# Kernel tuning notes

Hardware: AMD Instinct MI355X
Metric: run time of the kernel (lower is better)

Reference implementation:

```python
import jax, jax.numpy as jnp
import numpy as np

NKV = 8      # n_head_kv
G = 8        # n_head // n_head_kv
D = 64       # head_dim (hardcoded in source views)
NH = NKV * G # n_head = 64


def rotate_half(x):
    x1, x2 = x[..., : D // 2], x[..., D // 2:]
    return jnp.concatenate((-x2, x1), axis=-1)


def setup_inputs() -> dict:
    key = jax.random.key(0)
    ks = jax.random.split(key, 9)
    B, S, H = 2, 1024, 4096
    hidden_states = jax.random.normal(ks[0], (B, S, H), dtype=jnp.float32)
    alibi = jnp.zeros((B * NH, 1, S), dtype=jnp.float32)            # unused in this forward path
    attention_mask = jnp.zeros((B, 1, S, S), dtype=jnp.float32)      # unused (is_causal=True)
    cos = jax.random.uniform(ks[1], (S, D), dtype=jnp.float32, minval=-1.0, maxval=1.0)
    sin = jax.random.uniform(ks[2], (S, D), dtype=jnp.float32, minval=-1.0, maxval=1.0)
    wq = jax.random.normal(ks[3], (H, H), dtype=jnp.float32) * 0.02          # Linear weight (out, in)
    wk = jax.random.normal(ks[4], (NKV * D, H), dtype=jnp.float32) * 0.02
    wv = jax.random.normal(ks[5], (NKV * D, H), dtype=jnp.float32) * 0.02
    wd = jax.random.normal(ks[6], (H, H), dtype=jnp.float32) * 0.02          # dense weight
    return {"hidden_states": hidden_states, "alibi": alibi, "attention_mask": attention_mask,
            "cos": cos, "sin": sin, "wq": wq, "wk": wk, "wv": wv, "wd": wd}


def reference(hidden_states, alibi, attention_mask, cos, sin, wq, wk, wv, wd):
    B, S, H = hidden_states.shape
    # fused-style projections (Linear: x @ W.T, no bias)
    # q: [B, S, NKV, G, D] -> [B, NKV, G, S, D]; head h = kv_group*G + j (group-major, matches source rearrange)
    q = (hidden_states @ wq.T).reshape(B, S, NKV, G, D).transpose(0, 2, 3, 1, 4)
    k = (hidden_states @ wk.T).reshape(B, S, NKV, D).transpose(0, 2, 1, 3)   # [B, NKV, S, D]
    v = (hidden_states @ wv.T).reshape(B, S, NKV, D).transpose(0, 2, 1, 3)
    # RoPE (cos/sin broadcast over batch/head dims)
    q = q * cos + rotate_half(q) * sin
    k = k * cos + rotate_half(k) * sin
    # grouped-query attention without materializing broadcast K/V
    inv_norm = jnp.asarray(1.0 / np.sqrt(D), dtype=hidden_states.dtype)
    scores = jnp.einsum('bkgsd,bktd->bkgst', q, k) * inv_norm        # [B, NKV, G, S, S]
    causal = jnp.tril(jnp.ones((S, S), dtype=bool))
    neg = jnp.finfo(scores.dtype).min
    scores = jnp.where(causal, scores, scores + neg)
    probs = jax.nn.softmax(scores, axis=-1)
    out = jnp.einsum('bkgst,bktd->bkgsd', probs, v)                  # [B, NKV, G, S, D]
    out = out.reshape(B, NH, S, D).transpose(0, 2, 1, 3).reshape(B, S, NH * D)
    return out @ wd.T
```

## Files before the change

### kernel.cpp

```cpp
#include <hip/hip_runtime.h>
#include <hip/hip_bf16.h>
#include <cstdint>

typedef short short8 __attribute__((ext_vector_type(8)));
typedef __bf16 bf16x8 __attribute__((ext_vector_type(8)));
typedef float float4v __attribute__((ext_vector_type(4)));
typedef float float16v __attribute__((ext_vector_type(16)));

#define NKV 8
#define G 8
#define D 64
#define NH 64
#define BB 2
#define S 1024
#define H 4096
#define MROWS (BB*S)
#define NQKV (H + 2*NKV*D)

__device__ __forceinline__ unsigned short f2b(float f) {
    union { float f; uint32_t u; } v; v.f = f;
    uint32_t u = v.u;
    uint32_t r = (u + 0x7FFFu + ((u >> 16) & 1u)) >> 16;
    return (unsigned short)r;
}
__device__ __forceinline__ float b2f(unsigned short b) {
    union { float f; uint32_t u; } v; v.u = ((uint32_t)b) << 16;
    return v.f;
}

__device__ __forceinline__ void gload_lds16(const unsigned short* g, unsigned short* l) {
    __builtin_amdgcn_global_load_lds(
        (const __attribute__((address_space(1))) uint32_t*)g,
        (__attribute__((address_space(3))) uint32_t*)l, 16, 0, 0);
}

__global__ void cvt_all(const float* __restrict__ hs, const float* __restrict__ wq,
                        const float* __restrict__ wk, const float* __restrict__ wv,
                        const float* __restrict__ wd,
                        unsigned short* __restrict__ hs_b, unsigned short* __restrict__ wqkv_b,
                        unsigned short* __restrict__ wd_b) {
    const size_t N0 = (size_t)MROWS * H;
    const size_t N1 = (size_t)H * H;
    const size_t N2 = (size_t)512 * H;
    const size_t N3 = (size_t)512 * H;
    const size_t N4 = (size_t)H * H;
    const size_t total4 = (N0 + N1 + N2 + N3 + N4) / 4;
    size_t i = (size_t)blockIdx.x * blockDim.x + threadIdx.x;
    const size_t stride = (size_t)gridDim.x * blockDim.x;
    for (; i < total4; i += stride) {
        size_t e = i * 4;
        const float* s; unsigned short* d;
        if (e < N0)                { s = hs + e;                  d = hs_b + e; }
        else if (e < N0+N1)        { s = wq + (e-N0);             d = wqkv_b + (e-N0); }
        else if (e < N0+N1+N2)     { s = wk + (e-N0-N1);          d = wqkv_b + N1 + (e-N0-N1); }
        else if (e < N0+N1+N2+N3)  { s = wv + (e-N0-N1-N2);       d = wqkv_b + N1+N2 + (e-N0-N1-N2); }
        else                       { s = wd + (e-N0-N1-N2-N3);    d = wd_b + (e-N0-N1-N2-N3); }
        float4 f = *(const float4*)s;
        ushort4 o;
        o.x = f2b(f.x); o.y = f2b(f.y); o.z = f2b(f.z); o.w = f2b(f.w);
        *(ushort4*)d = o;
    }
}

template <int MODE>
__global__ __launch_bounds__(256) void gemm_nt(
    const unsigned short* __restrict__ A, const unsigned short* __restrict__ W,
    void* __restrict__ Cv, int M, int N, int K,
    const float* __restrict__ cosb, const float* __restrict__ sinb,
    unsigned short* __restrict__ qa, unsigned short* __restrict__ ka,
    unsigned short* __restrict__ vt) {
    __shared__ unsigned short sh[17408];
    unsigned short* As = sh;
    unsigned short* Bs = sh + 4096;
    const int bm = blockIdx.y * 128, bn = blockIdx.x * 128;
    const int tid = threadIdx.x;
    const int w = tid >> 6, lane = tid & 63;
    const int n32 = lane & 31, khalf = lane >> 5;
    const int wm = (w & 1) * 64, wn = (w >> 1) * 64;

    const int r0 = tid >> 2;
    const int c0 = (tid & 3) ^ ((r0 >> 2) & 3);
    const unsigned short* pA0 = A + (size_t)(bm + r0) * K + c0 * 8;
    const unsigned short* pA1 = A + (size_t)(bm + r0 + 64) * K + c0 * 8;
    const unsigned short* pW0 = W + (size_t)(bn + r0) * K + c0 * 8;
    const unsigned short* pW1 = W + (size_t)(bn + r0 + 64) * K + c0 * 8;
    unsigned short* Asl0 = As + tid * 8;
    unsigned short* Asl1 = As + 2048 + tid * 8;
    unsigned short* Bsl0 = Bs + tid * 8;
    unsigned short* Bsl1 = Bs + 2048 + tid * 8;

    const unsigned short* aP[2][2];
    const unsigned short* bP[2][2];
#pragma unroll
    for (int g = 0; g < 2; g++)
#pragma unroll
        for (int s = 0; s < 2; s++) {
            int cp = ((s << 1) | khalf) ^ ((n32 >> 2) & 3);
            aP[g][s] = &As[(wm + g * 32 + n32) * 32 + cp * 8];
            bP[g][s] = &Bs[(wn + g * 32 + n32) * 32 + cp * 8];
        }

    float16v acc[2][2] = {};

    const int iters = K >> 5;
    for (int it = 0; it < iters; ++it) {
        __syncthreads();
        gload_lds16(pA0, Asl0);
        gload_lds16(pA1, Asl1);
        gload_lds16(pW0, Bsl0);
        gload_lds16(pW1, Bsl1);
        pA0 += 32; pA1 += 32; pW0 += 32; pW1 += 32;
        __syncthreads();
        bf16x8 af[2][2], bf[2][2];
#pragma unroll
        for (int g = 0; g < 2; g++)
#pragma unroll
            for (int s = 0; s < 2; s++) {
                af[g][s] = *(const bf16x8*)aP[g][s];
                bf[g][s] = *(const bf16x8*)bP[g][s];
            }
#pragma unroll
        for (int s = 0; s < 2; s++)
#pragma unroll
            for (int mg = 0; mg < 2; mg++)
#pragma unroll
                for (int ng = 0; ng < 2; ng++)
                    acc[mg][ng] = __builtin_amdgcn_mfma_f32_32x32x16_bf16(
                        af[mg][s], bf[ng][s], acc[mg][ng], 0, 0, 0);
    }

    if (MODE == 0) {
#pragma unroll
        for (int mg = 0; mg < 2; mg++) {
#pragma unroll
            for (int ng = 0; ng < 2; ng++) {
                int gcol = bn + wn + ng * 32 + n32;
#pragma unroll
                for (int reg = 0; reg < 16; reg++) {
                    int grow = bm + wm + mg * 32 + (reg & 3) + 8 * (reg >> 2) + 4 * khalf;
                    ((float*)Cv)[(size_t)grow * N + gcol] = acc[mg][ng][reg];
                }
            }
        }
    } else {
        const int colbase = bn + wn;
        const float SCQ = 0.125f * 1.44269504089f;
        if (bn < H + 512) {
#pragma unroll
            for (int mg = 0; mg < 2; mg++) {
#pragma unroll
                for (int reg = 0; reg < 16; reg++) {
                    int grow = bm + wm + mg * 32 + (reg & 3) + 8 * (reg >> 2) + 4 * khalf;
                    int s = grow & 1023, b = grow >> 10;
                    float x0 = acc[mg][0][reg], x1 = acc[mg][1][reg];
                    float c0  = cosb[s * 64 + n32],      sn0 = sinb[s * 64 + n32];
                    float c1  = cosb[s * 64 + 32 + n32], sn1 = sinb[s * 64 + 32 + n32];
                    float y0 = x0 * c0 - x1 * sn0;
                    float y1 = x1 * c1 + x0 * sn1;
                    unsigned short* dp;
                    if (bn < H) {
                        y0 *= SCQ; y1 *= SCQ;
                        dp = qa + (size_t)(b * 64 + (colbase >> 6)) * (S * D) + s * 64 + n32;
                    } else {
                        dp = ka + (size_t)(b * 8 + ((colbase - H) >> 6)) * (S * D) + s * 64 + n32;
                    }
                    dp[0] = f2b(y0); dp[32] = f2b(y1);
                }
            }
        } else {
            __syncthreads();
#pragma unroll
            for (int mg = 0; mg < 2; mg++)
#pragma unroll
                for (int ng = 0; ng < 2; ng++)
#pragma unroll
                    for (int reg = 0; reg < 16; reg++) {
                        int cl = wn + ng * 32 + n32;
                        int rl = wm + mg * 32 + (reg & 3) + 8 * (reg >> 2) + 4 * khalf;
                        sh[cl * 136 + rl] = f2b(acc[mg][ng][reg]);
                    }
            __syncthreads();
            {
                const int bb = bm >> 10, s0 = bm & 1023;
                const int kv0 = (bn - (H + 512)) >> 6;
                const int cl = tid >> 1, shalf = (tid & 1) * 64;
                const int kv = kv0 + (cl >> 6), dd = cl & 63;
                unsigned short* dstp = vt + (size_t)(bb * 8 + kv) * (D * S)
                                          + (size_t)dd * S + s0 + shalf;
                const unsigned short* srcp = sh + cl * 136 + shalf;
#pragma unroll
                for (int j = 0; j < 8; j++)
                    *(short8*)(dstp + j * 8) = *(const short8*)(srcp + j * 8);
            }
        }
    }
}

__global__ __launch_bounds__(256) void attn_kernel(
    const unsigned short* __restrict__ qa, const unsigned short* __restrict__ ka,
    const unsigned short* __restrict__ vt, unsigned short* __restrict__ out) {
    __shared__ unsigned short Ps[4 * 16 * 72];
    const int p = blockIdx.x;
    const int yy = blockIdx.y;
    const int b = yy >> 5, kvh = (yy >> 2) & 7, gp = yy & 3;
    const int h0 = b * 64 + kvh * 8 + gp * 2;
    const int tid = threadIdx.x, w = tid >> 6, lane = tid & 63;
    const int col = lane & 15, quad = lane >> 4;
    const unsigned short* Kg = ka + (size_t)(b * NKV + kvh) * (S * D);
    const unsigned short* Vg = vt + (size_t)(b * NKV + kvh) * (D * S);
    float4v zero4 = {0.f, 0.f, 0.f, 0.f};

#pragma unroll
    for (int part = 0; part < 2; part++) {
        const int qt = part ? (15 - p) : p;
        const int qb = qt * 64;

        bf16x8 aq[2][2];
#pragma unroll
        for (int hd = 0; hd < 2; hd++)
#pragma unroll
            for (int c = 0; c < 2; c++)
                aq[hd][c] = *(const bf16x8*)&qa[(size_t)(h0 + hd) * (S * D) + (size_t)qb * D
                                               + (w * 16 + col) * 64 + c * 32 + quad * 8];

        float l_run[2][4];
        float4v o_acc[2][4];
#pragma unroll
        for (int hd = 0; hd < 2; hd++) {
#pragma unroll
            for (int r = 0; r < 4; r++) l_run[hd][r] = 0.f;
#pragma unroll
            for (int dg = 0; dg < 4; dg++) o_acc[hd][dg] = zero4;
        }

        for (int kt = 0; kt <= qt; kt++) {
            const int kb = kt * 64;
            bf16x8 bk[4][2], bv[4][2];
#pragma unroll
            for (int n16 = 0; n16 < 4; n16++) {
                const unsigned short* kr = &Kg[(size_t)(kb + n16 * 16 + col) * 64 + quad * 8];
                bk[n16][0] = *(const bf16x8*)kr;
                bk[n16][1] = *(const bf16x8*)(kr + 32);
            }
#pragma unroll
            for (int dg = 0; dg < 4; dg++) {
                const unsigned short* vr = &Vg[(size_t)(dg * 16 + col) * S + kb + quad * 8];
                bv[dg][0] = *(const bf16x8*)vr;
                bv[dg][1] = *(const bf16x8*)(vr + 32);
            }

#pragma unroll
            for (int hd = 0; hd < 2; hd++) {
                float4v sc[4];
                __builtin_amdgcn_s_setprio(1);
#pragma unroll
                for (int n16 = 0; n16 < 4; n16++) {
                    float4v a = __builtin_amdgcn_mfma_f32_16x16x32_bf16(aq[hd][0], bk[n16][0], zero4, 0, 0, 0);
                    sc[n16] = __builtin_amdgcn_mfma_f32_16x16x32_bf16(aq[hd][1], bk[n16][1], a, 0, 0, 0);
                }
                __builtin_amdgcn_s_setprio(0);
                if (kt == qt) {
#pragma unroll
                    for (int n16 = 0; n16 < 4; n16++) {
                        int keyl = n16 * 16 + col;
#pragma unroll
                        for (int r = 0; r < 4; r++) {
                            int qrl = w * 16 + quad * 4 + r;
                            sc[n16][r] = (keyl <= qrl) ? sc[n16][r] : -1e30f;
                        }
                    }
                }
#pragma unroll
                for (int n16 = 0; n16 < 4; n16++)
#pragma unroll
                    for (int r = 0; r < 4; r++) {
                        float pr = __builtin_amdgcn_exp2f(sc[n16][r]);
                        sc[n16][r] = pr;
                        l_run[hd][r] += pr;
                        Ps[w * 1152 + (quad * 4 + r) * 72 + n16 * 16 + col] = f2b(pr);
                    }
                bf16x8 ap[2];
#pragma unroll
                for (int c = 0; c < 2; c++)
                    ap[c] = *(const bf16x8*)&Ps[w * 1152 + col * 72 + c * 32 + quad * 8];
                __builtin_amdgcn_s_setprio(1);
#pragma unroll
                for (int dg = 0; dg < 4; dg++) {
                    float4v t = __builtin_amdgcn_mfma_f32_16x16x32_bf16(ap[0], bv[dg][0], o_acc[hd][dg], 0, 0, 0);
                    o_acc[hd][dg] = __builtin_amdgcn_mfma_f32_16x16x32_bf16(ap[1], bv[dg][1], t, 0, 0, 0);
                }
                __builtin_amdgcn_s_setprio(0);
            }
        }
#pragma unroll
        for (int hd = 0; hd < 2; hd++) {
            const int hcol = ((h0 + hd) & 63) * 64;
#pragma unroll
            for (int r = 0; r < 4; r++) {
                float lsum = l_run[hd][r];
#pragma unroll
                for (int off = 1; off < 16; off <<= 1) lsum += __shfl_xor(lsum, off);
                float inv = 1.f / lsum;
                int grow = b * S + qb + w * 16 + quad * 4 + r;
#pragma unroll
                for (int dg = 0; dg < 4; dg++)
                    out[(size_t)grow * H + hcol + dg * 16 + col] = f2b(o_acc[hd][dg][r] * inv);
            }
        }
    }
}

extern "C" void kernel_launch(void* const* d_in, const int* in_sizes, int n_in,
                              void* d_out, int out_size, void* d_ws, size_t ws_size,
                              hipStream_t stream) {
    const float* hs   = (const float*)d_in[0];
    const float* cosb = (const float*)d_in[3];
    const float* sinb = (const float*)d_in[4];
    const float* wq   = (const float*)d_in[5];
    const float* wk   = (const float*)d_in[6];
    const float* wv   = (const float*)d_in[7];
    const float* wd   = (const float*)d_in[8];

    char* p = (char*)d_ws;
    auto alloc = [&](size_t bytes) { char* r = p; p += (bytes + 255) & ~(size_t)255; return r; };
    unsigned short* wqkv_b = (unsigned short*)alloc((size_t)NQKV * H * 2);
    unsigned short* wd_b   = (unsigned short*)alloc((size_t)H * H * 2);
    unsigned short* qa     = (unsigned short*)alloc((size_t)BB * NH * S * D * 2);
    unsigned short* ka     = (unsigned short*)alloc((size_t)BB * NKV * S * D * 2);
    unsigned short* vt     = (unsigned short*)alloc((size_t)BB * NKV * S * D * 2);
    unsigned short* hs_b   = (unsigned short*)alloc((size_t)MROWS * H * 2);
    unsigned short* ao     = hs_b;

    cvt_all<<<4096, 256, 0, stream>>>(hs, wq, wk, wv, wd, hs_b, wqkv_b, wd_b);

    gemm_nt<1><<<dim3(NQKV / 128, MROWS / 128), 256, 0, stream>>>(
        hs_b, wqkv_b, nullptr, MROWS, NQKV, H, cosb, sinb, qa, ka, vt);
    attn_kernel<<<dim3(8, 64), 256, 0, stream>>>(qa, ka, vt, ao);
    gemm_nt<0><<<dim3(H / 128, MROWS / 128), 256, 0, stream>>>(
        ao, wd_b, d_out, MROWS, H, H, nullptr, nullptr, nullptr, nullptr, nullptr);
}
```

Baseline: 475.9 us.

## Share K/V tile loads across both paired query tiles in attention kernel

The attention kernel now walks a single key-tile loop for both of its paired query tiles (p and 15-p) instead of running two separate passes. Each K/V tile is loaded once and used by both query tiles, which roughly halves K/V global loads for the shorter tile. In exchange it keeps twice the Q fragments, accumulators and row sums live in registers. It also asks for 2 blocks per CU through launch bounds and swaps the manual bf16 rounding for the native conversion.

Result: no change. 473.2 us (-0.6%).

```diff
diff --git a/kernel.cpp b/kernel.cpp
--- a/kernel.cpp
+++ b/kernel.cpp
@@ -26,6 +26,10 @@
 __device__ __forceinline__ float b2f(unsigned short b) {
     union { float f; uint32_t u; } v; v.u = ((uint32_t)b) << 16;
     return v.f;
+}
+__device__ __forceinline__ unsigned short f2b_n(float f) {
+    union { __bf16 h; unsigned short u; } v; v.h = (__bf16)f;
+    return v.u;
 }
 
 __device__ __forceinline__ void gload_lds16(const unsigned short* g, unsigned short* l) {
@@ -196,7 +200,7 @@
     }
 }
 
-__global__ __launch_bounds__(256) void attn_kernel(
+__global__ __launch_bounds__(256, 2) void attn_kernel(
     const unsigned short* __restrict__ qa, const unsigned short* __restrict__ ka,
     const unsigned short* __restrict__ vt, unsigned short* __restrict__ out) {
     __shared__ unsigned short Ps[4 * 16 * 72];
@@ -210,56 +214,59 @@
     const unsigned short* Vg = vt + (size_t)(b * NKV + kvh) * (D * S);
     float4v zero4 = {0.f, 0.f, 0.f, 0.f};
 
-#pragma unroll
-    for (int part = 0; part < 2; part++) {
-        const int qt = part ? (15 - p) : p;
-        const int qb = qt * 64;
-
-        bf16x8 aq[2][2];
+    const int qt0 = p, qt1 = 15 - p;
+    const int qb[2] = {qt0 * 64, qt1 * 64};
+
+    bf16x8 aq[2][2][2];
+#pragma unroll
+    for (int part = 0; part < 2; part++)
 #pragma unroll
         for (int hd = 0; hd < 2; hd++)
 #pragma unroll
             for (int c = 0; c < 2; c++)
-                aq[hd][c] = *(const bf16x8*)&qa[(size_t)(h0 + hd) * (S * D) + (size_t)qb * D
-                                               + (w * 16 + col) * 64 + c * 32 + quad * 8];
-
-        float l_run[2][4];
-        float4v o_acc[2][4];
-#pragma unroll
-        for (int hd = 0; hd < 2; hd++) {
-#pragma unroll
-            for (int r = 0; r < 4; r++) l_run[hd][r] = 0.f;
-#pragma unroll
-            for (int dg = 0; dg < 4; dg++) o_acc[hd][dg] = zero4;
-        }
-
-        for (int kt = 0; kt <= qt; kt++) {
-            const int kb = kt * 64;
-            bf16x8 bk[4][2], bv[4][2];
-#pragma unroll
-            for (int n16 = 0; n16 < 4; n16++) {
-                const unsigned short* kr = &Kg[(size_t)(kb + n16 * 16 + col) * 64 + quad * 8];
-                bk[n16][0] = *(const bf16x8*)kr;
-                bk[n16][1] = *(const bf16x8*)(kr + 32);
-            }
-#pragma unroll
-            for (int dg = 0; dg < 4; dg++) {
-                const unsigned short* vr = &Vg[(size_t)(dg * 16 + col) * S + kb + quad * 8];
-                bv[dg][0] = *(const bf16x8*)vr;
-                bv[dg][1] = *(const bf16x8*)(vr + 32);
-            }
-
+                aq[part][hd][c] = *(const bf16x8*)&qa[(size_t)(h0 + hd) * (S * D)
+                                    + (size_t)qb[part] * D + (w * 16 + col) * 64 + c * 32 + quad * 8];
+
+    float l_run[2][2][4] = {};
+    float4v o_acc[2][2][4];
+#pragma unroll
+    for (int part = 0; part < 2; part++)
+#pragma unroll
+        for (int hd = 0; hd < 2; hd++)
+#pragma unroll
+            for (int dg = 0; dg < 4; dg++) o_acc[part][hd][dg] = zero4;
+
+    for (int kt = 0; kt <= qt1; kt++) {
+        const int kb = kt * 64;
+        bf16x8 bk[4][2], bv[4][2];
+#pragma unroll
+        for (int n16 = 0; n16 < 4; n16++) {
+            const unsigned short* kr = &Kg[(size_t)(kb + n16 * 16 + col) * 64 + quad * 8];
+            bk[n16][0] = *(const bf16x8*)kr;
+            bk[n16][1] = *(const bf16x8*)(kr + 32);
+        }
+#pragma unroll
+        for (int dg = 0; dg < 4; dg++) {
+            const unsigned short* vr = &Vg[(size_t)(dg * 16 + col) * S + kb + quad * 8];
+            bv[dg][0] = *(const bf16x8*)vr;
+            bv[dg][1] = *(const bf16x8*)(vr + 32);
+        }
+
+#pragma unroll
+        for (int part = 0; part < 2; part++) {
+            const int qtp = part ? qt1 : qt0;
+            if (kt > qtp) continue;
 #pragma unroll
             for (int hd = 0; hd < 2; hd++) {
                 float4v sc[4];
                 __builtin_amdgcn_s_setprio(1);
 #pragma unroll
                 for (int n16 = 0; n16 < 4; n16++) {
-                    float4v a = __builtin_amdgcn_mfma_f32_16x16x32_bf16(aq[hd][0], bk[n16][0], zero4, 0, 0, 0);
-                    sc[n16] = __builtin_amdgcn_mfma_f32_16x16x32_bf16(aq[hd][1], bk[n16][1], a, 0, 0, 0);
+                    float4v a = __builtin_amdgcn_mfma_f32_16x16x32_bf16(aq[part][hd][0], bk[n16][0], zero4, 0, 0, 0);
+                    sc[n16] = __builtin_amdgcn_mfma_f32_16x16x32_bf16(aq[part][hd][1], bk[n16][1], a, 0, 0, 0);
                 }
                 __builtin_amdgcn_s_setprio(0);
-                if (kt == qt) {
+                if (kt == qtp) {
 #pragma unroll
                     for (int n16 = 0; n16 < 4; n16++) {
                         int keyl = n16 * 16 + col;
@@ -276,8 +283,8 @@
                     for (int r = 0; r < 4; r++) {
                         float pr = __builtin_amdgcn_exp2f(sc[n16][r]);
                         sc[n16][r] = pr;
-                        l_run[hd][r] += pr;
-                        Ps[w * 1152 + (quad * 4 + r) * 72 + n16 * 16 + col] = f2b(pr);
+                        l_run[part][hd][r] += pr;
+                        Ps[w * 1152 + (quad * 4 + r) * 72 + n16 * 16 + col] = f2b_n(pr);
                     }
                 bf16x8 ap[2];
 #pragma unroll
@@ -286,28 +293,31 @@
                 __builtin_amdgcn_s_setprio(1);
 #pragma unroll
                 for (int dg = 0; dg < 4; dg++) {
-                    float4v t = __builtin_amdgcn_mfma_f32_16x16x32_bf16(ap[0], bv[dg][0], o_acc[hd][dg], 0, 0, 0);
-                    o_acc[hd][dg] = __builtin_amdgcn_mfma_f32_16x16x32_bf16(ap[1], bv[dg][1], t, 0, 0, 0);
+                    float4v t = __builtin_amdgcn_mfma_f32_16x16x32_bf16(ap[0], bv[dg][0], o_acc[part][hd][dg], 0, 0, 0);
+                    o_acc[part][hd][dg] = __builtin_amdgcn_mfma_f32_16x16x32_bf16(ap[1], bv[dg][1], t, 0, 0, 0);
                 }
                 __builtin_amdgcn_s_setprio(0);
             }
         }
+    }
+
+#pragma unroll
+    for (int part = 0; part < 2; part++)
 #pragma unroll
         for (int hd = 0; hd < 2; hd++) {
             const int hcol = ((h0 + hd) & 63) * 64;
 #pragma unroll
             for (int r = 0; r < 4; r++) {
-                float lsum = l_run[hd][r];
+                float lsum = l_run[part][hd][r];
 #pragma unroll
                 for (int off = 1; off < 16; off <<= 1) lsum += __shfl_xor(lsum, off);
                 float inv = 1.f / lsum;
-                int grow = b * S + qb + w * 16 + quad * 4 + r;
+                int grow = b * S + qb[part] + w * 16 + quad * 4 + r;
 #pragma unroll
                 for (int dg = 0; dg < 4; dg++)
-                    out[(size_t)grow * H + hcol + dg * 16 + col] = f2b(o_acc[hd][dg][r] * inv);
-            }
-        }
-    }
+                    out[(size_t)grow * H + hcol + dg * 16 + col] = f2b_n(o_acc[part][hd][dg][r] * inv);
+            }
+        }
 }
 
 extern "C" void kernel_launch(void* const* d_in, const int* in_sizes, int n_in,
```
